# Kernel tuning notes

Hardware: AMD Instinct MI355X
Metric: run time of the kernel (lower is better)

## Reference

```python
import jax, jax.numpy as jnp
import numpy as np

N_NODES = 2048
UNITS = 64
IN_DIM = 64
K_DIFF = 2  # max_diffusion_step


def _rw_norm_t(adj):
    # random-walk normalize D^{-1}(A+I), then transpose (as in forward())
    a = adj + jnp.eye(adj.shape[0], dtype=adj.dtype)
    d = jnp.sum(a, axis=1)
    d_inv = jnp.where(d > 0, 1.0 / jnp.where(d > 0, d, 1.0), 0.0)
    return (d_inv[:, None] * a).T


def _gconv(x_cat, adj_t, W, b):
    # x_cat: (B, N, F). Chebyshev-like diffusion: x0, A x0, 2 A x1 - x0, ...
    x0 = x_cat
    xs = [x0]
    x1 = jnp.einsum('nm,bmf->bnf', adj_t, x0)
    xs.append(x1)
    for _ in range(2, K_DIFF + 1):
        x2 = 2.0 * jnp.einsum('nm,bmf->bnf', adj_t, x1) - x0
        xs.append(x2)
        x0, x1 = x1, x2
    x = jnp.stack(xs, axis=-1)  # (B, N, F, K+1) -> matches torch permute(3,1,2,0)
    B, N, F, K = x.shape
    x = x.reshape(B * N, F * K)
    out = x @ W + b
    return out.reshape(B, N, -1)


def setup_inputs() -> dict:
    key = jax.random.key(0)
    ks = jax.random.split(key, 6)
    B = 64
    inputs = jax.random.normal(ks[0], (B, N_NODES * IN_DIM), dtype=jnp.float32)
    hx = jax.random.normal(ks[1], (B, N_NODES * UNITS), dtype=jnp.float32)
    adj = jax.random.uniform(ks[2], (N_NODES, N_NODES), dtype=jnp.float32)
    in_sz = IN_DIM + UNITS
    nm = K_DIFF + 1
    scale = float(np.sqrt(2.0 / (in_sz * nm + 2 * UNITS)))  # xavier-ish
    W_ru = jax.random.normal(ks[3], (in_sz * nm, 2 * UNITS), dtype=jnp.float32) * scale
    b_ru = jnp.ones((2 * UNITS,), dtype=jnp.float32)  # bias_start=1.0
    W_c = jax.random.normal(ks[4], (in_sz * nm, UNITS), dtype=jnp.float32) * scale
    b_c = jnp.zeros((UNITS,), dtype=jnp.float32)
    return {"inputs": inputs, "hx": hx, "adj": adj,
            "W_ru": W_ru, "b_ru": b_ru, "W_c": W_c, "b_c": b_c}


def reference(inputs, hx, adj, W_ru, b_ru, W_c, b_c):
    B = inputs.shape[0]
    x = inputs.reshape(B, N_NODES, IN_DIM)
    h = hx.reshape(B, N_NODES, UNITS)
    adj_t = _rw_norm_t(adj)
    # r/u gates via graph conv + sigmoid
    ru = jax.nn.sigmoid(_gconv(jnp.concatenate([x, h], axis=-1), adj_t, W_ru, b_ru))
    r, u = ru[..., :UNITS], ru[..., UNITS:]
    # candidate state
    c = jnp.tanh(_gconv(jnp.concatenate([x, r * h], axis=-1), adj_t, W_c, b_c))
    new_state = u * h + (1.0 - u) * c
    return new_state.reshape(B, N_NODES * UNITS)
```

## Files before the change

kernel.cpp:

```cpp
#include <hip/hip_runtime.h>
#include <math.h>

typedef __attribute__((ext_vector_type(8))) short short8;
typedef __attribute__((ext_vector_type(4))) float float4v;
typedef __attribute__((ext_vector_type(16))) float float16v;
typedef __attribute__((ext_vector_type(4))) unsigned short ushort4v;
typedef unsigned short u16;
typedef unsigned int u32;

#define NB 64
#define NN 2048
#define FD 128
#define UD 64
#define KT 384


__device__ __forceinline__ u16 f2bf(float f) {
    unsigned int u = __float_as_uint(f);
    u += 0x7fffu + ((u >> 16) & 1u);
    return (u16)(u >> 16);
}
__device__ __forceinline__ float bf2f(u16 s) {
    return __uint_as_float(((unsigned int)s) << 16);
}
__device__ __forceinline__ float sigmoidf_(float x) {
    return 1.0f / (1.0f + expf(-x));
}
__device__ __forceinline__ void gl2lds16(const u16* g, u16* l) {
    __builtin_amdgcn_global_load_lds((const __attribute__((address_space(1))) unsigned int*)g,
                                     (__attribute__((address_space(3))) unsigned int*)l,
                                     16, 0, 0);
}

__global__ void k_prep(const float* __restrict__ adj, float* __restrict__ d_inv,
                       const float* __restrict__ W_ru, u16* __restrict__ Wru,
                       const float* __restrict__ W_c,  u16* __restrict__ Wc,
                       const float* __restrict__ x, const float* __restrict__ h,
                       u16* __restrict__ X0f, u16* __restrict__ X0m) {
    __shared__ u16 T[128 * 136];
    int bid = blockIdx.x;
    int t = threadIdx.x;
    if (bid < 2048) {
        int m = bid;
        const float4v* row = (const float4v*)(adj + (size_t)m * NN);
        float s = 0.f;
        for (int i = t; i < NN / 4; i += 256) {
            float4v v = row[i];
            s += v.x + v.y + v.z + v.w;
        }
        float* red = (float*)T;
        for (int off = 32; off; off >>= 1) s += __shfl_down(s, off, 64);
        if ((t & 63) == 0) red[t >> 6] = s;
        __syncthreads();
        if (t == 0) {
            float tt = red[0] + red[1] + red[2] + red[3] + 1.0f;
            d_inv[m] = 1.0f / tt;
        }
        return;
    }
    if (bid < 2336) {
        const float* W; u16* Wt; int OD, idx;
        if (bid < 2240) { W = W_ru; Wt = Wru; OD = FD; idx = (bid - 2048) * 256 + t; }
        else            { W = W_c;  Wt = Wc;  OD = UD; idx = (bid - 2240) * 256 + t; }
        if (idx >= KT * OD) return;
        int o  = idx % OD;
        int kp = idx / OD;
        int kd = kp >> 7, f = kp & 127;
        float v;
        if (kd == 0)      v = W[(size_t)(f * 3 + 0) * OD + o] - W[(size_t)(f * 3 + 2) * OD + o];
        else if (kd == 1) v = W[(size_t)(f * 3 + 1) * OD + o];
        else              v = 2.0f * W[(size_t)(f * 3 + 2) * OD + o];
        size_t dst = ((size_t)(o >> 5) * 12 + (kp >> 5)) * 1024 + (((kp >> 3) & 3) * 32 + (o & 31)) * 8 + (kp & 7);
        Wt[dst] = f2bf(v);
        return;
    }
    int rb = bid - 2336;
    int m0 = (rb & 15) * 128;
    int b  = rb >> 4;
    const float* srcs[2] = { x + (size_t)b * (NN * 64), h + (size_t)b * (NN * 64) };
    for (int s = 0; s < 2; ++s) {
        const float* src = srcs[s];
        for (int p = 0; p < 8; ++p) {
            int idx = t + 256 * p;
            int mi = idx >> 4;
            int f4 = idx & 15;
            float4v v = *(const float4v*)(src + (size_t)(m0 + mi) * 64 + f4 * 4);
            float vv[4] = {v.x, v.y, v.z, v.w};
#pragma unroll
            for (int j = 0; j < 4; ++j)
                T[(s * 64 + f4 * 4 + j) * 136 + mi] = f2bf(vv[j]);
        }
    }
    __syncthreads();
#pragma unroll
    for (int p = 0; p < 8; ++p) {
        int S = t + 256 * p;
        int fgl = S >> 9, kgl = (S >> 7) & 3, s = S & 127;
        int c = s >> 5, r = s & 31;
        short8 v = *(const short8*)(T + (fgl * 32 + r) * 136 + kgl * 32 + c * 8);
        *(short8*)(X0f + ((size_t)(b * 4 + fgl) * 64 + (m0 >> 5) + kgl) * 1024 + s * 8) = v;
    }
#pragma unroll
    for (int p = 0; p < 8; ++p) {
        int S = t + 256 * p;
        int fc = S >> 7;
        int mi = S & 127;
        short8 v;
#pragma unroll
        for (int e = 0; e < 8; ++e) v[e] = (short)T[(fc * 8 + e) * 136 + mi];
        size_t dst = ((size_t)(b * 64 + (m0 >> 5) + (mi >> 5)) * 4 + (fc >> 2)) * 1024
                     + ((fc & 3) * 32 + (mi & 31)) * 8;
        *(short8*)(X0m + dst) = v;
    }
}

__global__ void k_adjT(const float* __restrict__ adj, const float* __restrict__ d_inv,
                       u16* __restrict__ adjT) {
    __shared__ u16 T[64 * 72];
    int m0 = blockIdx.x * 64;
    int n0 = blockIdx.y * 64;
    int t = threadIdx.x;
    for (int p = 0; p < 4; ++p) {
        int idx = t + 256 * p;
        int i  = idx >> 4;
        int n4 = idx & 15;
        int m = m0 + i;
        float4v v = *(const float4v*)(adj + (size_t)m * NN + n0 + n4 * 4);
        float di = d_inv[m];
        float vv[4] = {v.x, v.y, v.z, v.w};
#pragma unroll
        for (int j = 0; j < 4; ++j) {
            int n = n0 + n4 * 4 + j;
            float a = vv[j] + ((m == n) ? 1.0f : 0.0f);
            T[(n4 * 4 + j) * 72 + i] = f2bf(a * di);
        }
    }
    __syncthreads();
#pragma unroll
    for (int p = 0; p < 2; ++p) {
        int S = t + 256 * p;
        int rgl = S >> 8, kgl = (S >> 7) & 1, s = S & 127;
        int c = s >> 5, r = s & 31;
        short8 v = *(const short8*)(T + (rgl * 32 + r) * 72 + kgl * 32 + c * 8);
        *(short8*)(adjT + ((size_t)((n0 >> 5) + rgl) * 64 + (m0 >> 5) + kgl) * 1024 + s * 8) = v;
    }
}

template<int HAS_F>
__global__ __launch_bounds__(512, 2)
void k_gemm256(const u16* __restrict__ Ap, const u16* __restrict__ Bc,
               u16* __restrict__ outF, u16* __restrict__ outM) {
    __shared__ __align__(16) u16 SM[49152];
    int bid = blockIdx.x;
    int wxcd = bid >> 3;
    int cb = (bid & 7) * 4 + (wxcd & 3);
    int nb = wxcd >> 2;
    int n0 = nb * 256, c0 = cb * 256;
    int t = threadIdx.x;
    int wave = t >> 6, lane = t & 63;
    int wx = wave >> 2;
    int wy = wave & 3;
    int ln = lane & 31, hi = lane >> 5;

    const u16* gA[2];
    const u16* gB[2];
    int la[2], lb[2];
#pragma unroll
    for (int i = 0; i < 2; ++i) {
        int idx = i * 512 + t;
        int p = idx >> 7, s = idx & 127;
        gA[i] = Bc + ((size_t)((c0 >> 5) + p) * 64) * 1024 + s * 8;
        gB[i] = Ap + ((size_t)((n0 >> 5) + p) * 64) * 1024 + s * 8;
        la[i] = idx * 8;
        lb[i] = 8192 + idx * 8;
    }

    float16v acc[4][2];
#pragma unroll
    for (int mt = 0; mt < 4; ++mt)
#pragma unroll
        for (int nt = 0; nt < 2; ++nt)
#pragma unroll
            for (int e = 0; e < 16; ++e) acc[mt][nt][e] = 0.f;

#pragma unroll
    for (int i = 0; i < 2; ++i) { gl2lds16(gA[i], SM + la[i]); gl2lds16(gB[i], SM + lb[i]); }
#pragma unroll
    for (int i = 0; i < 2; ++i) { gl2lds16(gA[i] + 1024, SM + 16384 + la[i]); gl2lds16(gB[i] + 1024, SM + 16384 + lb[i]); }
    asm volatile("s_waitcnt vmcnt(4)" ::: "memory");
    __builtin_amdgcn_s_barrier();
    __builtin_amdgcn_sched_barrier(0);

    int rdA = wx * 4096 + lane * 8;
    int rdB = 8192 + wy * 2048 + lane * 8;

    int cur = 0;
    for (int kt = 0; kt < 64; ++kt) {
        u16* buf = SM + cur * 16384;
        int stg = cur + 2; if (stg >= 3) stg -= 3;
        u16* sbuf = SM + stg * 16384;
        size_t ko = (size_t)(kt + 2) * 1024;

        short8 fa0[4], fb0[2], fa1[4], fb1[2];
#pragma unroll
        for (int mt = 0; mt < 4; ++mt) fa0[mt] = *(const short8*)(buf + rdA + mt * 1024);
#pragma unroll
        for (int nt = 0; nt < 2; ++nt) fb0[nt] = *(const short8*)(buf + rdB + nt * 1024);
        if (kt < 62) {
#pragma unroll
            for (int i = 0; i < 2; ++i) gl2lds16(gA[i] + ko, sbuf + la[i]);
#pragma unroll
            for (int i = 0; i < 2; ++i) gl2lds16(gB[i] + ko, sbuf + lb[i]);
        }
#pragma unroll
        for (int mt = 0; mt < 4; ++mt) fa1[mt] = *(const short8*)(buf + rdA + mt * 1024 + 512);

        __builtin_amdgcn_s_setprio(1);
#pragma unroll
        for (int mt = 0; mt < 4; ++mt)
#pragma unroll
            for (int nt = 0; nt < 2; ++nt)
                acc[mt][nt] = __builtin_amdgcn_mfma_f32_32x32x16_bf16(fa0[mt], fb0[nt], acc[mt][nt], 0, 0, 0);
        __builtin_amdgcn_s_setprio(0);

#pragma unroll
        for (int nt = 0; nt < 2; ++nt) fb1[nt] = *(const short8*)(buf + rdB + nt * 1024 + 512);

        __builtin_amdgcn_s_setprio(1);
#pragma unroll
        for (int mt = 0; mt < 4; ++mt)
#pragma unroll
            for (int nt = 0; nt < 2; ++nt)
                acc[mt][nt] = __builtin_amdgcn_mfma_f32_32x32x16_bf16(fa1[mt], fb1[nt], acc[mt][nt], 0, 0, 0);
        __builtin_amdgcn_s_setprio(0);

        if (kt < 62) asm volatile("s_waitcnt vmcnt(4)" ::: "memory");
        else         asm volatile("s_waitcnt vmcnt(0)" ::: "memory");
        __builtin_amdgcn_s_barrier();
        __builtin_amdgcn_sched_barrier(0);

        cur = (cur == 2) ? 0 : cur + 1;
    }

    int batch0 = cb * 2 + wx;
#pragma unroll
    for (int mt = 0; mt < 4; ++mt) {
#pragma unroll
        for (int nt = 0; nt < 2; ++nt) {
            int mg = (n0 >> 5) + wy * 2 + nt;
            size_t pbase = ((size_t)(batch0 * 64 + mg) * 4 + mt) * 1024;
#pragma unroll
            for (int eq = 0; eq < 4; ++eq) {
                ushort4v pk;
#pragma unroll
                for (int r = 0; r < 4; ++r) pk[r] = f2bf(acc[mt][nt][eq * 4 + r]);
                *(ushort4v*)(outM + pbase + (eq * 32 + ln) * 8 + 4 * hi) = pk;
            }
        }
    }

    if (HAS_F) {
#pragma unroll
        for (int p = 0; p < 2; ++p) {
            __syncthreads();
            if ((wy >> 1) == p) {
#pragma unroll
                for (int mt = 0; mt < 4; ++mt)
#pragma unroll
                    for (int nt = 0; nt < 2; ++nt)
#pragma unroll
                        for (int e = 0; e < 16; ++e) {
                            int cl = wx * 128 + mt * 32 + 4 * hi + 8 * (e >> 2) + (e & 3);
                            int nl = (wy & 1) * 64 + nt * 32 + ln;
                            SM[cl * 136 + nl] = f2bf(acc[mt][nt][e]);
                        }
            }
            __syncthreads();
#pragma unroll
            for (int j = 0; j < 8; ++j) {
                int S = t + 512 * j;
                int col = S >> 4, nd8 = S & 15;
                short8 v = *(const short8*)(SM + col * 136 + nd8 * 8);
                int gn = n0 + p * 128 + nd8 * 8;
                size_t dst = ((size_t)((c0 >> 5) + (col >> 5)) * 64 + (gn >> 5)) * 1024
                             + (size_t)((((gn >> 3) & 3) * 32 + (col & 31))) * 8;
                *(short8*)(outF + dst) = v;
            }
        }
    }
}

template<int FG>
__global__ __launch_bounds__(256, 4)
void k_gemm(const u16* __restrict__ A, const u16* __restrict__ Bc,
            u16* __restrict__ outF, u16* __restrict__ outM, int cBlocks) {
    __shared__ u16 SM[16384];
    u16* A0 = SM;            u16* A1 = SM + 4096;
    u16* B0 = SM + 8192;     u16* B1 = SM + 12288;

    int id = blockIdx.x + cBlocks * blockIdx.y;
    int band = cBlocks >> 3;
    int g = id & 7, s = id >> 3;
    int cb = g * band + (s % band);
    int nb = s / band;
    int c0 = cb * 128;
    int n0 = nb * 128;

    int t = threadIdx.x;
    int wave = t >> 6, lane = t & 63;
    int wy = wave & 1, wx = wave >> 1;
    int ln = lane & 31, hi = lane >> 5;
    int l16 = lane * 8;

    const u16* gaP[2];
    const u16* gbP[2];
#pragma unroll
    for (int i = 0; i < 2; ++i) {
        int T = t + 256 * i;
        gaP[i] = A  + ((size_t)((n0 >> 5) + (T >> 7)) * 64) * 1024 + (size_t)(T & 127) * 8;
        gbP[i] = Bc + ((size_t)((c0 >> 5) + (T >> 7)) * 64) * 1024 + (size_t)(T & 127) * 8;
    }

    float16v acc[2][2];
#pragma unroll
    for (int i = 0; i < 2; ++i)
#pragma unroll
        for (int j = 0; j < 2; ++j)
#pragma unroll
            for (int e = 0; e < 16; ++e) acc[i][j][e] = 0.f;

#pragma unroll
    for (int i = 0; i < 2; ++i) { gl2lds16(gaP[i], A0 + (t + 256 * i) * 8); gl2lds16(gbP[i], B0 + (t + 256 * i) * 8); }

#pragma unroll 2
    for (int it = 0; it < 64; ++it) {
        u16* Ac = (it & 1) ? A1 : A0;
        u16* Bs = (it & 1) ? B1 : B0;
        __syncthreads();
        if (it + 1 < 64) {
            int ko = (it + 1) * 1024;
            u16* An = (it & 1) ? A0 : A1;
            u16* Bn = (it & 1) ? B0 : B1;
#pragma unroll
            for (int i = 0; i < 2; ++i) { gl2lds16(gaP[i] + ko, An + (t + 256 * i) * 8); gl2lds16(gbP[i] + ko, Bn + (t + 256 * i) * 8); }
        }
        short8 fa[2][2], fb[2][2];
#pragma unroll
        for (int ks = 0; ks < 2; ++ks) {
#pragma unroll
            for (int mt = 0; mt < 2; ++mt)
                fa[ks][mt] = *(const short8*)(Bs + ((wx * 2 + mt) * 2 + ks) * 512 + l16);
#pragma unroll
            for (int nt = 0; nt < 2; ++nt)
                fb[ks][nt] = *(const short8*)(Ac + ((wy * 2 + nt) * 2 + ks) * 512 + l16);
        }
#pragma unroll
        for (int ks = 0; ks < 2; ++ks)
#pragma unroll
            for (int mt = 0; mt < 2; ++mt)
#pragma unroll
                for (int nt = 0; nt < 2; ++nt)
                    acc[mt][nt] = __builtin_amdgcn_mfma_f32_32x32x16_bf16(fa[ks][mt], fb[ks][nt], acc[mt][nt], 0, 0, 0);
    }

#pragma unroll
    for (int mt = 0; mt < 2; ++mt) {
#pragma unroll
        for (int nt = 0; nt < 2; ++nt) {
            int mg = (n0 >> 5) + wy * 2 + nt;
            int batch = (FG == 4) ? cb : (2 * cb + wx);
            int fg = (FG == 4) ? (wx * 2 + mt) : mt;
            size_t pbase = ((size_t)(batch * 64 + mg) * FG + fg) * 1024;
#pragma unroll
            for (int eq = 0; eq < 4; ++eq) {
                ushort4v pk;
#pragma unroll
                for (int r = 0; r < 4; ++r) pk[r] = f2bf(acc[mt][nt][eq * 4 + r]);
                *(ushort4v*)(outM + pbase + (eq * 32 + ln) * 8 + 4 * hi) = pk;
            }
        }
    }

    if (outF) {
        __syncthreads();
#pragma unroll
        for (int p = 0; p < 2; ++p) {
            if (p) __syncthreads();
            if (wx == p) {
#pragma unroll
                for (int mt = 0; mt < 2; ++mt)
#pragma unroll
                    for (int nt = 0; nt < 2; ++nt)
#pragma unroll
                        for (int e = 0; e < 16; ++e) {
                            int cl = mt * 32 + 4 * hi + 8 * (e >> 2) + (e & 3);
                            int nl = wy * 64 + nt * 32 + ln;
                            SM[cl * 136 + nl] = f2bf(acc[mt][nt][e]);
                        }
            }
            __syncthreads();
#pragma unroll
            for (int pp = 0; pp < 4; ++pp) {
                int S = t + 256 * pp;
                int rgl = S >> 9, kgl = (S >> 7) & 3, sl = S & 127;
                int c = sl >> 5, r = sl & 31;
                short8 v = *(const short8*)(SM + (rgl * 32 + r) * 136 + kgl * 32 + c * 8);
                size_t gaddr = ((size_t)((c0 >> 5) + p * 2 + rgl) * 64 + (n0 >> 5) + kgl) * 1024 + sl * 8;
                *(short8*)(outF + gaddr) = v;
            }
        }
    }
}

__global__ __launch_bounds__(256, 3)
void k_proj_ru(const u16* __restrict__ X0m, const u16* __restrict__ X1m, const u16* __restrict__ Ym,
               const u16* __restrict__ Wp, const float* __restrict__ bias, const float* __restrict__ hx,
               u16* __restrict__ RH0f, u16* __restrict__ RH0m, u16* __restrict__ Ut) {
    __shared__ u16 SM[16384];
    u16 *Xa = SM, *Xb = SM + 4096, *Wa = SM + 8192, *Wb = SM + 12288;
    int mb = blockIdx.x, b = blockIdx.y;
    int m0 = mb * 128, mg0 = mb * 4;
    int t = threadIdx.x, wave = t >> 6, lane = t & 63;
    int wx = wave & 1, wyy = wave >> 1;
    int ln = lane & 31, hi = lane >> 5;
    const u16* Xs[3] = {X0m, X1m, Ym};
    int p0 = t >> 7, s0 = t & 127;

    float16v acc[2][2];
#pragma unroll
    for (int i = 0; i < 2; ++i)
#pragma unroll
        for (int j = 0; j < 2; ++j)
#pragma unroll
            for (int e = 0; e < 16; ++e) acc[i][j][e] = 0.f;

    gl2lds16(Xs[0] + ((size_t)((b * 64 + mg0 + p0) * 4)) * 1024 + s0 * 8, Xa + t * 8);
    gl2lds16(Xs[0] + ((size_t)((b * 64 + mg0 + p0 + 2) * 4)) * 1024 + s0 * 8, Xa + (t + 256) * 8);
    gl2lds16(Wp + ((size_t)(p0 * 12)) * 1024 + s0 * 8, Wa + t * 8);
    gl2lds16(Wp + ((size_t)((p0 + 2) * 12)) * 1024 + s0 * 8, Wa + (t + 256) * 8);

    for (int kq = 0; kq < 12; ++kq) {
        u16* Xc = (kq & 1) ? Xb : Xa;
        u16* Wc = (kq & 1) ? Wb : Wa;
        __syncthreads();
        if (kq + 1 < 12) {
            int k2 = kq + 1, kd = k2 >> 2, kg = k2 & 3;
            u16* Xn = (kq & 1) ? Xa : Xb;
            u16* Wn = (kq & 1) ? Wa : Wb;
            const u16* xb = Xs[kd];
            gl2lds16(xb + ((size_t)((b * 64 + mg0 + p0) * 4 + kg)) * 1024 + s0 * 8, Xn + t * 8);
            gl2lds16(xb + ((size_t)((b * 64 + mg0 + p0 + 2) * 4 + kg)) * 1024 + s0 * 8, Xn + (t + 256) * 8);
            gl2lds16(Wp + ((size_t)(p0 * 12 + k2)) * 1024 + s0 * 8, Wn + t * 8);
            gl2lds16(Wp + ((size_t)((p0 + 2) * 12 + k2)) * 1024 + s0 * 8, Wn + (t + 256) * 8);
        }
        short8 fa[2][2], fb[2][2];
#pragma unroll
        for (int ks = 0; ks < 2; ++ks) {
#pragma unroll
            for (int mt = 0; mt < 2; ++mt)
                fa[ks][mt] = *(const short8*)(Xc + ((wx * 2 + mt) * 2 + ks) * 512 + lane * 8);
#pragma unroll
            for (int nt = 0; nt < 2; ++nt)
                fb[ks][nt] = *(const short8*)(Wc + ((wyy * 2 + nt) * 2 + ks) * 512 + lane * 8);
        }
#pragma unroll
        for (int ks = 0; ks < 2; ++ks)
#pragma unroll
            for (int mt = 0; mt < 2; ++mt)
#pragma unroll
                for (int nt = 0; nt < 2; ++nt)
                    acc[mt][nt] = __builtin_amdgcn_mfma_f32_32x32x16_bf16(fa[ks][mt], fb[ks][nt], acc[mt][nt], 0, 0, 0);
    }
    __syncthreads();
    if (wyy == 0) {
#pragma unroll
        for (int mt = 0; mt < 2; ++mt)
#pragma unroll
            for (int nt = 0; nt < 2; ++nt) {
                int o = nt * 32 + ln;
                float bo = bias[o];
                u16 vals[16];
#pragma unroll
                for (int e = 0; e < 16; ++e) {
                    int ml = wx * 64 + mt * 32 + 4 * hi + 8 * (e >> 2) + (e & 3);
                    float sg = sigmoidf_(acc[mt][nt][e] + bo);
                    float hh = hx[((size_t)b * NN + m0 + ml) * 64 + o];
                    vals[e] = f2bf(sg * hh);
                    SM[ml * 76 + o] = vals[e];
                }
#pragma unroll
                for (int eq = 0; eq < 4; ++eq) {
                    ushort4v pk;
#pragma unroll
                    for (int r = 0; r < 4; ++r) pk[r] = vals[eq * 4 + r];
                    size_t addr = ((size_t)(b * 2 + nt) * 64 + mg0 + wx * 2 + mt) * 1024 + (eq * 32 + ln) * 8 + 4 * hi;
                    *(ushort4v*)(RH0f + addr) = pk;
                }
            }
    } else {
#pragma unroll
        for (int mt = 0; mt < 2; ++mt)
#pragma unroll
            for (int nt = 0; nt < 2; ++nt) {
                int og = nt * 32 + ln;
                float bo = bias[64 + og];
#pragma unroll
                for (int e = 0; e < 16; ++e) {
                    int ml = wx * 64 + mt * 32 + 4 * hi + 8 * (e >> 2) + (e & 3);
                    Ut[((size_t)b * NN + m0 + ml) * 64 + og] = f2bf(sigmoidf_(acc[mt][nt][e] + bo));
                }
            }
    }
    __syncthreads();
#pragma unroll
    for (int j = 0; j < 4; ++j) {
        int C = t + 256 * j;
        int p = C >> 7, sl = C & 127;
        int mgl = p >> 1, ug = p & 1;
        int cq = sl >> 5, r = sl & 31;
        short8 v = *(const short8*)(SM + (mgl * 32 + r) * 76 + ug * 32 + cq * 8);
        *(short8*)(RH0m + ((size_t)((b * 64 + mg0 + mgl) * 2 + ug)) * 1024 + sl * 8) = v;
    }
}

__global__ __launch_bounds__(256, 4)
void k_proj_c(const u16* __restrict__ X0m, const u16* __restrict__ X1m, const u16* __restrict__ Ym,
              const u16* __restrict__ RH0m, const u16* __restrict__ RH1m, const u16* __restrict__ Zm,
              const u16* __restrict__ Wp, const float* __restrict__ bias,
              const float* __restrict__ hx, const u16* __restrict__ Ut,
              float* __restrict__ out) {
    __shared__ u16 SM[12288];
    u16 *Xa = SM, *Xb = SM + 4096, *Wa = SM + 8192, *Wb = SM + 10240;
    int mb = blockIdx.x, b = blockIdx.y;
    int m0 = mb * 128, mg0 = mb * 4;
    int t = threadIdx.x, wave = t >> 6, lane = t & 63;
    int wx = wave & 1, wyy = wave >> 1;
    int ln = lane & 31, hi = lane >> 5;
    const u16* Xs[3] = {X0m, X1m, Ym};
    const u16* Rs[3] = {RH0m, RH1m, Zm};
    int p0 = t >> 7, s0 = t & 127;

    float16v acc[2];
#pragma unroll
    for (int i = 0; i < 2; ++i)
#pragma unroll
        for (int e = 0; e < 16; ++e) acc[i][e] = 0.f;

    gl2lds16(Xs[0] + ((size_t)((b * 64 + mg0 + p0) * 4)) * 1024 + s0 * 8, Xa + t * 8);
    gl2lds16(Xs[0] + ((size_t)((b * 64 + mg0 + p0 + 2) * 4)) * 1024 + s0 * 8, Xa + (t + 256) * 8);
    gl2lds16(Wp + ((size_t)(p0 * 12)) * 1024 + s0 * 8, Wa + t * 8);

    for (int kq = 0; kq < 12; ++kq) {
        u16* Xc = (kq & 1) ? Xb : Xa;
        u16* Wc = (kq & 1) ? Wb : Wa;
        __syncthreads();
        if (kq + 1 < 12) {
            int k2 = kq + 1, kd = k2 >> 2, fb2 = (k2 & 3) * 32;
            u16* Xn = (kq & 1) ? Xa : Xb;
            u16* Wn = (kq & 1) ? Wa : Wb;
            const u16* mat; size_t pb0, pb1;
            if (fb2 < 64) {
                mat = Xs[kd];
                pb0 = ((size_t)((b * 64 + mg0 + p0) * 4 + (fb2 >> 5))) * 1024;
                pb1 = ((size_t)((b * 64 + mg0 + p0 + 2) * 4 + (fb2 >> 5))) * 1024;
            } else {
                mat = Rs[kd];
                pb0 = ((size_t)((b * 64 + mg0 + p0) * 2 + ((fb2 >> 5) - 2))) * 1024;
                pb1 = ((size_t)((b * 64 + mg0 + p0 + 2) * 2 + ((fb2 >> 5) - 2))) * 1024;
            }
            gl2lds16(mat + pb0 + s0 * 8, Xn + t * 8);
            gl2lds16(mat + pb1 + s0 * 8, Xn + (t + 256) * 8);
            gl2lds16(Wp + ((size_t)(p0 * 12 + k2)) * 1024 + s0 * 8, Wn + t * 8);
        }
        short8 fa[2][2], fbg[2];
#pragma unroll
        for (int ks = 0; ks < 2; ++ks) {
#pragma unroll
            for (int mt = 0; mt < 2; ++mt)
                fa[ks][mt] = *(const short8*)(Xc + ((wx * 2 + mt) * 2 + ks) * 512 + lane * 8);
            fbg[ks] = *(const short8*)(Wc + (wyy * 2 + ks) * 512 + lane * 8);
        }
#pragma unroll
        for (int ks = 0; ks < 2; ++ks)
#pragma unroll
            for (int mt = 0; mt < 2; ++mt)
                acc[mt] = __builtin_amdgcn_mfma_f32_32x32x16_bf16(fa[ks][mt], fbg[ks], acc[mt], 0, 0, 0);
    }
    int o = wyy * 32 + ln;
    float bo = bias[o];
#pragma unroll
    for (int mt = 0; mt < 2; ++mt)
#pragma unroll
        for (int e = 0; e < 16; ++e) {
            int ml = wx * 64 + mt * 32 + 4 * hi + 8 * (e >> 2) + (e & 3);
            size_t idx = ((size_t)b * NN + m0 + ml) * 64 + o;
            float c = tanhf(acc[mt][e] + bo);
            float u = bf2f(Ut[idx]);
            float hh = hx[idx];
            out[idx] = u * hh + (1.0f - u) * c;
        }
}

extern "C" void kernel_launch(void* const* d_in, const int* in_sizes, int n_in,
                              void* d_out, int out_size, void* d_ws, size_t ws_size,
                              hipStream_t stream) {
    const float* x    = (const float*)d_in[0];
    const float* hx   = (const float*)d_in[1];
    const float* adj  = (const float*)d_in[2];
    const float* W_ru = (const float*)d_in[3];
    const float* b_ru = (const float*)d_in[4];
    const float* W_c  = (const float*)d_in[5];
    const float* b_c  = (const float*)d_in[6];
    float* out = (float*)d_out;

    char* ws = (char*)d_ws;
    size_t off = 0;
    auto alloc = [&](size_t bytes) -> void* {
        void* p = ws + off;
        off += (bytes + 255) & ~(size_t)255;
        return p;
    };
    float* d_inv = (float*)alloc((size_t)NN * 4);
    u16* adjT = (u16*)alloc((size_t)NN * NN * 2);
    u16* Wru  = (u16*)alloc((size_t)FD * KT * 2);
    u16* Wc   = (u16*)alloc((size_t)UD * KT * 2);
    u16* X0f = (u16*)alloc((size_t)NB * FD * NN * 2);
    u16* X1f = (u16*)alloc((size_t)NB * FD * NN * 2);
    u16* X0m = (u16*)alloc((size_t)NB * FD * NN * 2);
    u16* X1m = (u16*)alloc((size_t)NB * FD * NN * 2);
    u16* Ym  = (u16*)alloc((size_t)NB * FD * NN * 2);
    u16* RH0m = (u16*)alloc((size_t)NB * UD * NN * 2);
    u16* RH1m = (u16*)alloc((size_t)NB * UD * NN * 2);
    u16* Zm   = (u16*)alloc((size_t)NB * UD * NN * 2);
    u16* Ut   = (u16*)alloc((size_t)NB * UD * NN * 2);
    u16* RH0f = X0f;
    u16* RH1f = X1f;

    k_prep<<<dim3(3360), dim3(256), 0, stream>>>(adj, d_inv, W_ru, Wru, W_c, Wc, x, hx, X0f, X0m);
    k_adjT<<<dim3(32, 32), dim3(256), 0, stream>>>(adj, d_inv, adjT);
    k_gemm256<1><<<dim3(256), dim3(512), 0, stream>>>(adjT, X0f, X1f, X1m);
    k_gemm256<0><<<dim3(256), dim3(512), 0, stream>>>(adjT, X1f, nullptr, Ym);
    k_proj_ru<<<dim3(16, NB), dim3(256), 0, stream>>>(X0m, X1m, Ym, Wru, b_ru, hx, RH0f, RH0m, Ut);
    k_gemm<2><<<dim3(32, 16), dim3(256), 0, stream>>>(adjT, RH0f, RH1f, RH1m, 32);
    k_gemm<2><<<dim3(32, 16), dim3(256), 0, stream>>>(adjT, RH1f, nullptr, Zm, 32);
    k_proj_c<<<dim3(16, NB), dim3(256), 0, stream>>>(X0m, X1m, Ym, RH0m, RH1m, Zm, Wc, b_c, hx, Ut, out);
}
```

Before: 448.5 us.

## Replace direct global-to-LDS loads with register-staged double-buffered prefetch in GEMM

The GEMM main loop no longer uses direct global-to-LDS copies. It now loads each k-tile into registers one step ahead, using two alternating register sets, and writes them into a triple-buffered LDS ring before the MFMA work. The aim is to hide global latency behind compute and avoid the vmcnt waits on the async LDS path. In exchange it uses more VGPRs for the staging registers, which could hurt occupancy at 2 blocks per CU, and it adds explicit LDS store traffic and lgkmcnt waits.

```diff
diff --git a/kernel.cpp b/kernel.cpp
--- a/kernel.cpp
+++ b/kernel.cpp
@@ -146,6 +146,52 @@
     }
 }
 
+#define GSTEP(KT, W0, W1, W2, W3, L0, L1, L2, L3)                              \
+  {                                                                            \
+    if ((KT) + 3 < 64) {                                                       \
+      size_t ko = (size_t)((KT) + 3) * 1024;                                   \
+      L0 = *(const short8*)(gA[0] + ko);                                       \
+      L1 = *(const short8*)(gA[1] + ko);                                       \
+      L2 = *(const short8*)(gB[0] + ko);                                       \
+      L3 = *(const short8*)(gB[1] + ko);                                       \
+    }                                                                          \
+    __builtin_amdgcn_sched_barrier(0);                                         \
+    if ((KT) + 2 < 64) {                                                       \
+      u16* wb = SM + bW * 16384;                                               \
+      *(short8*)(wb + la[0]) = W0;                                             \
+      *(short8*)(wb + la[1]) = W1;                                             \
+      *(short8*)(wb + lb[0]) = W2;                                             \
+      *(short8*)(wb + lb[1]) = W3;                                             \
+    }                                                                          \
+    u16* rb_ = SM + bR * 16384;                                                \
+    short8 fa[4], fb[2];                                                       \
+    _Pragma("unroll") for (int mt = 0; mt < 4; ++mt)                           \
+      fa[mt] = *(const short8*)(rb_ + rdA + mt * 1024);                        \
+    _Pragma("unroll") for (int nt = 0; nt < 2; ++nt)                           \
+      fb[nt] = *(const short8*)(rb_ + rdB + nt * 1024);                        \
+    __builtin_amdgcn_s_setprio(1);                                             \
+    _Pragma("unroll") for (int mt = 0; mt < 4; ++mt)                           \
+      _Pragma("unroll") for (int nt = 0; nt < 2; ++nt)                         \
+        acc[mt][nt] = __builtin_amdgcn_mfma_f32_32x32x16_bf16(fa[mt], fb[nt], acc[mt][nt], 0, 0, 0); \
+    __builtin_amdgcn_s_setprio(0);                                             \
+    _Pragma("unroll") for (int mt = 0; mt < 4; ++mt)                           \
+      fa[mt] = *(const short8*)(rb_ + rdA + mt * 1024 + 512);                  \
+    _Pragma("unroll") for (int nt = 0; nt < 2; ++nt)                           \
+      fb[nt] = *(const short8*)(rb_ + rdB + nt * 1024 + 512);                  \
+    __builtin_amdgcn_s_setprio(1);                                             \
+    _Pragma("unroll") for (int mt = 0; mt < 4; ++mt)                           \
+      _Pragma("unroll") for (int nt = 0; nt < 2; ++nt)                         \
+        acc[mt][nt] = __builtin_amdgcn_mfma_f32_32x32x16_bf16(fa[mt], fb[nt], acc[mt][nt], 0, 0, 0); \
+    __builtin_amdgcn_s_setprio(0);                                             \
+    asm volatile("s_waitcnt lgkmcnt(0)" ::: "memory");                         \
+    if ((KT) < 63) {                                                           \
+      __builtin_amdgcn_s_barrier();                                            \
+      __builtin_amdgcn_sched_barrier(0);                                       \
+    }                                                                          \
+    bR = (bR == 2) ? 0 : bR + 1;                                               \
+    bW = (bW == 2) ? 0 : bW + 1;                                               \
+  }
+
 template<int HAS_F>
 __global__ __launch_bounds__(512, 2)
 void k_gemm256(const u16* __restrict__ Ap, const u16* __restrict__ Bc,
@@ -183,63 +229,29 @@
 #pragma unroll
             for (int e = 0; e < 16; ++e) acc[mt][nt][e] = 0.f;
 
-#pragma unroll
-    for (int i = 0; i < 2; ++i) { gl2lds16(gA[i], SM + la[i]); gl2lds16(gB[i], SM + lb[i]); }
-#pragma unroll
-    for (int i = 0; i < 2; ++i) { gl2lds16(gA[i] + 1024, SM + 16384 + la[i]); gl2lds16(gB[i] + 1024, SM + 16384 + lb[i]); }
-    asm volatile("s_waitcnt vmcnt(4)" ::: "memory");
+    int rdA = wx * 4096 + lane * 8;
+    int rdB = 8192 + wy * 2048 + lane * 8;
+
+    short8 PA0, PA1, PA2, PA3, QB0, QB1, QB2, QB3;
+    PA0 = *(const short8*)(gA[0]);        PA1 = *(const short8*)(gA[1]);
+    PA2 = *(const short8*)(gB[0]);        PA3 = *(const short8*)(gB[1]);
+    QB0 = *(const short8*)(gA[0] + 1024); QB1 = *(const short8*)(gA[1] + 1024);
+    QB2 = *(const short8*)(gB[0] + 1024); QB3 = *(const short8*)(gB[1] + 1024);
+    *(short8*)(SM + la[0]) = PA0; *(short8*)(SM + la[1]) = PA1;
+    *(short8*)(SM + lb[0]) = PA2; *(short8*)(SM + lb[1]) = PA3;
+    asm volatile("s_waitcnt lgkmcnt(0)" ::: "memory");
+    PA0 = *(const short8*)(gA[0] + 2048); PA1 = *(const short8*)(gA[1] + 2048);
+    PA2 = *(const short8*)(gB[0] + 2048); PA3 = *(const short8*)(gB[1] + 2048);
+    *(short8*)(SM + 16384 + la[0]) = QB0; *(short8*)(SM + 16384 + la[1]) = QB1;
+    *(short8*)(SM + 16384 + lb[0]) = QB2; *(short8*)(SM + 16384 + lb[1]) = QB3;
+    asm volatile("s_waitcnt lgkmcnt(0)" ::: "memory");
     __builtin_amdgcn_s_barrier();
     __builtin_amdgcn_sched_barrier(0);
 
-    int rdA = wx * 4096 + lane * 8;
-    int rdB = 8192 + wy * 2048 + lane * 8;
-
-    int cur = 0;
-    for (int kt = 0; kt < 64; ++kt) {
-        u16* buf = SM + cur * 16384;
-        int stg = cur + 2; if (stg >= 3) stg -= 3;
-        u16* sbuf = SM + stg * 16384;
-        size_t ko = (size_t)(kt + 2) * 1024;
-
-        short8 fa0[4], fb0[2], fa1[4], fb1[2];
-#pragma unroll
-        for (int mt = 0; mt < 4; ++mt) fa0[mt] = *(const short8*)(buf + rdA + mt * 1024);
-#pragma unroll
-        for (int nt = 0; nt < 2; ++nt) fb0[nt] = *(const short8*)(buf + rdB + nt * 1024);
-        if (kt < 62) {
-#pragma unroll
-            for (int i = 0; i < 2; ++i) gl2lds16(gA[i] + ko, sbuf + la[i]);
-#pragma unroll
-            for (int i = 0; i < 2; ++i) gl2lds16(gB[i] + ko, sbuf + lb[i]);
-        }
-#pragma unroll
-        for (int mt = 0; mt < 4; ++mt) fa1[mt] = *(const short8*)(buf + rdA + mt * 1024 + 512);
-
-        __builtin_amdgcn_s_setprio(1);
-#pragma unroll
-        for (int mt = 0; mt < 4; ++mt)
-#pragma unroll
-            for (int nt = 0; nt < 2; ++nt)
-                acc[mt][nt] = __builtin_amdgcn_mfma_f32_32x32x16_bf16(fa0[mt], fb0[nt], acc[mt][nt], 0, 0, 0);
-        __builtin_amdgcn_s_setprio(0);
-
-#pragma unroll
-        for (int nt = 0; nt < 2; ++nt) fb1[nt] = *(const short8*)(buf + rdB + nt * 1024 + 512);
-
-        __builtin_amdgcn_s_setprio(1);
-#pragma unroll
-        for (int mt = 0; mt < 4; ++mt)
-#pragma unroll
-            for (int nt = 0; nt < 2; ++nt)
-                acc[mt][nt] = __builtin_amdgcn_mfma_f32_32x32x16_bf16(fa1[mt], fb1[nt], acc[mt][nt], 0, 0, 0);
-        __builtin_amdgcn_s_setprio(0);
-
-        if (kt < 62) asm volatile("s_waitcnt vmcnt(4)" ::: "memory");
-        else         asm volatile("s_waitcnt vmcnt(0)" ::: "memory");
-        __builtin_amdgcn_s_barrier();
-        __builtin_amdgcn_sched_barrier(0);
-
-        cur = (cur == 2) ? 0 : cur + 1;
+    int bR = 0, bW = 2;
+    for (int i = 0; i < 32; ++i) {
+        GSTEP(2 * i,     PA0, PA1, PA2, PA3, QB0, QB1, QB2, QB3);
+        GSTEP(2 * i + 1, QB0, QB1, QB2, QB3, PA0, PA1, PA2, PA3);
     }
 
     int batch0 = cb * 2 + wx;
```

New measurement: 441.0 us. No clear change (-1.7%).
